# Optimization experiments

Hardware: AMD Instinct MI355X
Metric: run time of the kernel (lower is better)

Reference implementation:

```python
import jax, jax.numpy as jnp
import numpy as np

EPS = 1e-12  # matches torch F.normalize default


def _l2norm_c(x):
    # normalize along channel dim (axis=1) of [B,C,H,W]
    n = jnp.sqrt(jnp.sum(x * x, axis=1, keepdims=True))
    return x / jnp.maximum(n, EPS)


def setup_inputs() -> dict:
    key = jax.random.key(0)
    ks = jax.random.split(key, 6)
    B, C, H, W = 2, 256, 64, 64
    return {
        "sv": jax.random.normal(ks[0], (B, 1, H, W), dtype=jnp.float32),
        "si": jax.random.normal(ks[1], (B, 1, H, W), dtype=jnp.float32),
        "sf": jax.random.normal(ks[2], (B, 1, H, W), dtype=jnp.float32),
        "dv": jax.random.normal(ks[3], (B, C, H, W), dtype=jnp.float32),
        "di": jax.random.normal(ks[4], (B, C, H, W), dtype=jnp.float32),
        "df": jax.random.normal(ks[5], (B, C, H, W), dtype=jnp.float32),
    }


def reference(sv, si, sf, dv, di, df):
    # keypoint score loss: L1(sf, max(sv, si))
    kp = jnp.mean(jnp.abs(sf - jnp.maximum(sv, si)))
    # descriptor loss: L1(df, (dv+di)/2)
    desc = jnp.mean(jnp.abs(df - (dv + di) * 0.5))
    # match loss (dense): normalize along C, full correlation volumes, L1
    a = _l2norm_c(dv)
    b = _l2norm_c(di)
    c = _l2norm_c(df)
    sim_ab = jnp.einsum('bchw,bcij->bhwij', a, b)  # [B,H,W,H,W]
    sim_ac = jnp.einsum('bchw,bcij->bhwij', a, c)
    match = jnp.mean(jnp.abs(sim_ac - sim_ab))
    return kp + desc + match
```

## Files before the change

### kernel.cpp

```cpp
#include <hip/hip_runtime.h>
#include <hip/hip_bf16.h>
#include <math.h>

#define BB 2
#define CC 256
#define HWN 4096
#define PPB 8
#define CCP 260


typedef __attribute__((ext_vector_type(4))) int   intx4;
typedef __attribute__((ext_vector_type(8))) int   intx8;
typedef __attribute__((ext_vector_type(4))) float floatx4;

__device__ __forceinline__ unsigned short f2bf(float f) {
    union { float f; unsigned u; } v; v.f = f;
    unsigned r = v.u + 0x7FFF + ((v.u >> 16) & 1);
    return (unsigned short)(r >> 16);
}

__device__ __forceinline__ float bf2f(unsigned short h) {
    union { unsigned u; float f; } v; v.u = ((unsigned)h) << 16;
    return v.f;
}

__global__ __launch_bounds__(256) void prep_kernel(
    const float* __restrict__ sv, const float* __restrict__ si,
    const float* __restrict__ sf, const float* __restrict__ dv,
    const float* __restrict__ di, const float* __restrict__ df,
    unsigned char* __restrict__ Af8, unsigned char* __restrict__ Df8,
    float* __restrict__ pk, float* __restrict__ pd)
{
    __shared__ unsigned short lv[PPB][CCP];
    __shared__ unsigned short li[PPB][CCP];
    __shared__ unsigned short lf[PPB][CCP];
    __shared__ float ssq[3][PPB];
    __shared__ float inv[3][PPB];
    __shared__ float sdesc;

    const int b   = blockIdx.x / (HWN / PPB);
    const int p0  = (blockIdx.x % (HWN / PPB)) * PPB;
    const int tid = threadIdx.x;
    const int q   = tid & 1;
    const int c0  = (tid >> 1) * 2;

    if (tid < 3 * PPB) ((float*)ssq)[tid] = 0.0f;
    if (tid == 0) sdesc = 0.0f;
    __syncthreads();

    const size_t rbase = ((size_t)b * CC + c0) * HWN + p0 + q * 4;
    const floatx4 v0 = *(const floatx4*)(dv + rbase);
    const floatx4 v1 = *(const floatx4*)(dv + rbase + HWN);
    const floatx4 i0 = *(const floatx4*)(di + rbase);
    const floatx4 i1 = *(const floatx4*)(di + rbase + HWN);
    const floatx4 f0 = *(const floatx4*)(df + rbase);
    const floatx4 f1 = *(const floatx4*)(df + rbase + HWN);

    float sqv[4], sqi[4], sqf[4], descp = 0.f;
    #pragma unroll
    for (int k = 0; k < 4; ++k) {
        sqv[k] = v0[k] * v0[k] + v1[k] * v1[k];
        sqi[k] = i0[k] * i0[k] + i1[k] * i1[k];
        sqf[k] = f0[k] * f0[k] + f1[k] * f1[k];
        descp += fabsf(f0[k] - 0.5f * (v0[k] + i0[k]))
               + fabsf(f1[k] - 0.5f * (v1[k] + i1[k]));
        const int p = q * 4 + k;
        *(unsigned*)&lv[p][c0] = (unsigned)f2bf(v0[k]) | ((unsigned)f2bf(v1[k]) << 16);
        *(unsigned*)&li[p][c0] = (unsigned)f2bf(i0[k]) | ((unsigned)f2bf(i1[k]) << 16);
        *(unsigned*)&lf[p][c0] = (unsigned)f2bf(f0[k]) | ((unsigned)f2bf(f1[k]) << 16);
    }

    #pragma unroll
    for (int off = 2; off < 64; off <<= 1) {
        #pragma unroll
        for (int k = 0; k < 4; ++k) {
            sqv[k] += __shfl_down(sqv[k], off);
            sqi[k] += __shfl_down(sqi[k], off);
            sqf[k] += __shfl_down(sqf[k], off);
        }
    }
    if ((tid & 63) < 2) {
        #pragma unroll
        for (int k = 0; k < 4; ++k) {
            atomicAdd(&ssq[0][q * 4 + k], sqv[k]);
            atomicAdd(&ssq[1][q * 4 + k], sqi[k]);
            atomicAdd(&ssq[2][q * 4 + k], sqf[k]);
        }
    }

    #pragma unroll
    for (int off = 32; off > 0; off >>= 1) descp += __shfl_down(descp, off);
    if ((tid & 63) == 0) atomicAdd(&sdesc, descp);

    if (tid < 64) {
        float kpv = 0.f;
        if (tid < PPB) {
            const size_t sidx = (size_t)b * HWN + p0 + tid;
            kpv = fabsf(sf[sidx] - fmaxf(sv[sidx], si[sidx]));
        }
        kpv += __shfl_down(kpv, 4);
        kpv += __shfl_down(kpv, 2);
        kpv += __shfl_down(kpv, 1);
        if (tid == 0) pk[blockIdx.x] = kpv;
    }
    __syncthreads();

    if (tid < 3 * PPB) {
        const float s = ((float*)ssq)[tid];
        ((float*)inv)[tid] = 1.0f / fmaxf(sqrtf(s), 1e-12f);
    }
    __syncthreads();

    if (tid == 0) pd[blockIdx.x] = sdesc;

    int* Ao = (int*)(Af8 + (size_t)b * HWN * CC);
    int* Do = (int*)(Df8 + (size_t)b * HWN * CC);
    const int obase = (p0 >> 4) * 1024 + (p0 & 8) * 8;
    #pragma unroll
    for (int s = 0; s < 2; ++s) {
        const int i  = tid + s * 256;
        const int kb = i >> 6, rem = i & 63;
        const int px = rem >> 3, cg = rem & 7;
        const int cs = kb * 32 + cg * 4;
        const float ia = inv[0][px], ibv = inv[1][px], ic = inv[2][px];
        float a0 = bf2f(lv[px][cs + 0]) * ia, a1 = bf2f(lv[px][cs + 1]) * ia;
        float a2 = bf2f(lv[px][cs + 2]) * ia, a3 = bf2f(lv[px][cs + 3]) * ia;
        float d0 = bf2f(lf[px][cs + 0]) * ic - bf2f(li[px][cs + 0]) * ibv;
        float d1 = bf2f(lf[px][cs + 1]) * ic - bf2f(li[px][cs + 1]) * ibv;
        float d2 = bf2f(lf[px][cs + 2]) * ic - bf2f(li[px][cs + 2]) * ibv;
        float d3 = bf2f(lf[px][cs + 3]) * ic - bf2f(li[px][cs + 3]) * ibv;
        int wa = __builtin_amdgcn_cvt_pk_fp8_f32(a0, a1, 0, false);
        wa     = __builtin_amdgcn_cvt_pk_fp8_f32(a2, a3, wa, true);
        int wd = __builtin_amdgcn_cvt_pk_fp8_f32(d0, d1, 0, false);
        wd     = __builtin_amdgcn_cvt_pk_fp8_f32(d2, d3, wd, true);
        const int oidx = obase + kb * 128 + px * 8 + cg;
        Ao[oidx] = wa;
        Do[oidx] = wd;
    }
}

__global__ __launch_bounds__(256) void gemm_abs_kernel(
    const unsigned char* __restrict__ Af8,
    const unsigned char* __restrict__ Df8,
    float* __restrict__ pg)
{
    const int b    = blockIdx.z;
    const int tid  = threadIdx.x;
    const int wave = tid >> 6;
    const int lane = tid & 63;
    const int wr   = wave >> 1, wc = wave & 1;
    const int mg0  = blockIdx.x * 8 + wr * 4;
    const int ng0  = blockIdx.y * 8 + wc * 4;

    const unsigned char* Ab = Af8 + (size_t)b * HWN * CC;
    const unsigned char* Db = Df8 + (size_t)b * HWN * CC;
    const int lofs = (lane >> 4) * 512 + (lane & 15) * 32;

    intx4 a[4][2][2], bb[4][2][2];
    #pragma unroll
    for (int mi = 0; mi < 4; ++mi)
        #pragma unroll
        for (int ks = 0; ks < 2; ++ks) {
            const unsigned char* pa = Ab + (size_t)(mg0 + mi) * 4096
                                    + ks * 2048 + lofs;
            a[mi][ks][0] = *(const intx4*)(pa);
            a[mi][ks][1] = *(const intx4*)(pa + 16);
        }
    #pragma unroll
    for (int ni = 0; ni < 4; ++ni)
        #pragma unroll
        for (int ks = 0; ks < 2; ++ks) {
            const unsigned char* pb = Db + (size_t)(ng0 + ni) * 4096
                                    + ks * 2048 + lofs;
            bb[ni][ks][0] = *(const intx4*)(pb);
            bb[ni][ks][1] = *(const intx4*)(pb + 16);
        }

    floatx4 accf[4][4];
    #pragma unroll
    for (int mi = 0; mi < 4; ++mi)
        #pragma unroll
        for (int ni = 0; ni < 4; ++ni)
            accf[mi][ni] = (floatx4){0.f, 0.f, 0.f, 0.f};

    #pragma unroll
    for (int ks = 0; ks < 2; ++ks)
        #pragma unroll
        for (int mi = 0; mi < 4; ++mi) {
            const intx8 a8 = __builtin_shufflevector(
                a[mi][ks][0], a[mi][ks][1], 0, 1, 2, 3, 4, 5, 6, 7);
            #pragma unroll
            for (int ni = 0; ni < 4; ++ni) {
                const intx8 b8 = __builtin_shufflevector(
                    bb[ni][ks][0], bb[ni][ks][1], 0, 1, 2, 3, 4, 5, 6, 7);
                accf[mi][ni] = __builtin_amdgcn_mfma_scale_f32_16x16x128_f8f6f4(
                    a8, b8, accf[mi][ni],
                    0, 0,
                    0, 0x7F7F7F7F,
                    0, 0x7F7F7F7F);
            }
        }

    float s = 0.f;
    #pragma unroll
    for (int mi = 0; mi < 4; ++mi)
        #pragma unroll
        for (int ni = 0; ni < 4; ++ni)
            #pragma unroll
            for (int r = 0; r < 4; ++r)
                s += fabsf(accf[mi][ni][r]);
    #pragma unroll
    for (int off = 32; off > 0; off >>= 1) s += __shfl_down(s, off);
    if (lane == 0) {
        const int flat = blockIdx.x + 32 * (blockIdx.y + 32 * blockIdx.z);
        pg[flat * 4 + wave] = s;
    }
}

__global__ __launch_bounds__(256) void final_kernel(
    const float* __restrict__ pg, const float* __restrict__ pk,
    const float* __restrict__ pd, float* __restrict__ out)
{
    __shared__ float ws[4];
    const int t = threadIdx.x;
    float s = 0.f;
    #pragma unroll
    for (int i = 0; i < 32; ++i)
        s += pg[t + i * 256];
    s *= (1.0f / 33554432.0f);
    float kd = 0.f;
    #pragma unroll
    for (int i = 0; i < 4; ++i)
        kd += pk[t + i * 256] * (1.0f / 8192.0f)
            + pd[t + i * 256] * (1.0f / 2097152.0f);
    s += kd;
    #pragma unroll
    for (int off = 32; off > 0; off >>= 1) s += __shfl_down(s, off);
    if ((t & 63) == 0) ws[t >> 6] = s;
    __syncthreads();
    if (t == 0) out[0] = ws[0] + ws[1] + ws[2] + ws[3];
}

extern "C" void kernel_launch(void* const* d_in, const int* in_sizes, int n_in,
                              void* d_out, int out_size, void* d_ws, size_t ws_size,
                              hipStream_t stream) {
    const float* sv = (const float*)d_in[0];
    const float* si = (const float*)d_in[1];
    const float* sf = (const float*)d_in[2];
    const float* dv = (const float*)d_in[3];
    const float* di = (const float*)d_in[4];
    const float* df = (const float*)d_in[5];

    unsigned char* Af8 = (unsigned char*)d_ws;
    unsigned char* Df8 = Af8 + (size_t)BB * HWN * CC;
    float* pg = (float*)(Df8 + (size_t)BB * HWN * CC);
    float* pk = pg + 8192;
    float* pd = pk + 1024;

    prep_kernel<<<dim3(BB * (HWN / PPB)), 256, 0, stream>>>(
        sv, si, sf, dv, di, df, Af8, Df8, pk, pd);
    gemm_abs_kernel<<<dim3(HWN / 128, HWN / 128, BB), 256, 0, stream>>>(
        Af8, Df8, pg);
    final_kernel<<<1, 256, 0, stream>>>(pg, pk, pd, (float*)d_out);
}
```

Baseline: 107.1 us.

## Widen GEMM tile to 128x256 and double pixels per prep block

The GEMM block now covers 256 columns instead of 128, with each wave holding a 4x8 accumulator grid. B fragments are streamed per column inside the k loop, so each A fragment is reused across twice as many MFMAs and the grid is halved. The prep kernel processes 16 pixels per block with each thread handling two channel halves, writing full 16-pixel output tiles. The partial-sum buffers and the final reduction are resized to match. Doubling the accumulators raises register pressure, which may reduce occupancy or cause spills.

```diff
diff --git a/kernel.cpp b/kernel.cpp
--- a/kernel.cpp
+++ b/kernel.cpp
@@ -5,7 +5,7 @@
 #define BB 2
 #define CC 256
 #define HWN 4096
-#define PPB 8
+#define PPB 16
 #define CCP 260
 
 
@@ -41,51 +41,53 @@
     const int b   = blockIdx.x / (HWN / PPB);
     const int p0  = (blockIdx.x % (HWN / PPB)) * PPB;
     const int tid = threadIdx.x;
-    const int q   = tid & 1;
-    const int c0  = (tid >> 1) * 2;
+    const int tp  = tid & 3;
+    const int c0  = (tid >> 2) * 2;
 
     if (tid < 3 * PPB) ((float*)ssq)[tid] = 0.0f;
     if (tid == 0) sdesc = 0.0f;
     __syncthreads();
 
-    const size_t rbase = ((size_t)b * CC + c0) * HWN + p0 + q * 4;
-    const floatx4 v0 = *(const floatx4*)(dv + rbase);
-    const floatx4 v1 = *(const floatx4*)(dv + rbase + HWN);
-    const floatx4 i0 = *(const floatx4*)(di + rbase);
-    const floatx4 i1 = *(const floatx4*)(di + rbase + HWN);
-    const floatx4 f0 = *(const floatx4*)(df + rbase);
-    const floatx4 f1 = *(const floatx4*)(df + rbase + HWN);
-
-    float sqv[4], sqi[4], sqf[4], descp = 0.f;
-    #pragma unroll
-    for (int k = 0; k < 4; ++k) {
-        sqv[k] = v0[k] * v0[k] + v1[k] * v1[k];
-        sqi[k] = i0[k] * i0[k] + i1[k] * i1[k];
-        sqf[k] = f0[k] * f0[k] + f1[k] * f1[k];
-        descp += fabsf(f0[k] - 0.5f * (v0[k] + i0[k]))
-               + fabsf(f1[k] - 0.5f * (v1[k] + i1[k]));
-        const int p = q * 4 + k;
-        *(unsigned*)&lv[p][c0] = (unsigned)f2bf(v0[k]) | ((unsigned)f2bf(v1[k]) << 16);
-        *(unsigned*)&li[p][c0] = (unsigned)f2bf(i0[k]) | ((unsigned)f2bf(i1[k]) << 16);
-        *(unsigned*)&lf[p][c0] = (unsigned)f2bf(f0[k]) | ((unsigned)f2bf(f1[k]) << 16);
-    }
-
-    #pragma unroll
-    for (int off = 2; off < 64; off <<= 1) {
+    float sq[3][4] = {};
+    float descp = 0.f;
+    #pragma unroll
+    for (int h = 0; h < 2; ++h) {
+        const int ch = c0 + h * 128;
+        const size_t rbase = ((size_t)b * CC + ch) * HWN + p0 + tp * 4;
+        const floatx4 v0 = *(const floatx4*)(dv + rbase);
+        const floatx4 v1 = *(const floatx4*)(dv + rbase + HWN);
+        const floatx4 i0 = *(const floatx4*)(di + rbase);
+        const floatx4 i1 = *(const floatx4*)(di + rbase + HWN);
+        const floatx4 f0 = *(const floatx4*)(df + rbase);
+        const floatx4 f1 = *(const floatx4*)(df + rbase + HWN);
         #pragma unroll
         for (int k = 0; k < 4; ++k) {
-            sqv[k] += __shfl_down(sqv[k], off);
-            sqi[k] += __shfl_down(sqi[k], off);
-            sqf[k] += __shfl_down(sqf[k], off);
-        }
-    }
-    if ((tid & 63) < 2) {
-        #pragma unroll
-        for (int k = 0; k < 4; ++k) {
-            atomicAdd(&ssq[0][q * 4 + k], sqv[k]);
-            atomicAdd(&ssq[1][q * 4 + k], sqi[k]);
-            atomicAdd(&ssq[2][q * 4 + k], sqf[k]);
-        }
+            sq[0][k] += v0[k] * v0[k] + v1[k] * v1[k];
+            sq[1][k] += i0[k] * i0[k] + i1[k] * i1[k];
+            sq[2][k] += f0[k] * f0[k] + f1[k] * f1[k];
+            descp += fabsf(f0[k] - 0.5f * (v0[k] + i0[k]))
+                   + fabsf(f1[k] - 0.5f * (v1[k] + i1[k]));
+            const int p = tp * 4 + k;
+            *(unsigned*)&lv[p][ch] = (unsigned)f2bf(v0[k]) | ((unsigned)f2bf(v1[k]) << 16);
+            *(unsigned*)&li[p][ch] = (unsigned)f2bf(i0[k]) | ((unsigned)f2bf(i1[k]) << 16);
+            *(unsigned*)&lf[p][ch] = (unsigned)f2bf(f0[k]) | ((unsigned)f2bf(f1[k]) << 16);
+        }
+    }
+
+    #pragma unroll
+    for (int off = 4; off < 64; off <<= 1) {
+        #pragma unroll
+        for (int j = 0; j < 3; ++j)
+            #pragma unroll
+            for (int k = 0; k < 4; ++k)
+                sq[j][k] += __shfl_down(sq[j][k], off);
+    }
+    if ((tid & 63) < 4) {
+        #pragma unroll
+        for (int j = 0; j < 3; ++j)
+            #pragma unroll
+            for (int k = 0; k < 4; ++k)
+                atomicAdd(&ssq[j][tp * 4 + k], sq[j][k]);
     }
 
     #pragma unroll
@@ -98,6 +100,7 @@
             const size_t sidx = (size_t)b * HWN + p0 + tid;
             kpv = fabsf(sf[sidx] - fmaxf(sv[sidx], si[sidx]));
         }
+        kpv += __shfl_down(kpv, 8);
         kpv += __shfl_down(kpv, 4);
         kpv += __shfl_down(kpv, 2);
         kpv += __shfl_down(kpv, 1);
@@ -115,13 +118,14 @@
 
     int* Ao = (int*)(Af8 + (size_t)b * HWN * CC);
     int* Do = (int*)(Df8 + (size_t)b * HWN * CC);
-    const int obase = (p0 >> 4) * 1024 + (p0 & 8) * 8;
-    #pragma unroll
-    for (int s = 0; s < 2; ++s) {
-        const int i  = tid + s * 256;
-        const int kb = i >> 6, rem = i & 63;
-        const int px = rem >> 3, cg = rem & 7;
-        const int cs = kb * 32 + cg * 4;
+    const int obase = (p0 >> 4) * 1024;
+    #pragma unroll
+    for (int s = 0; s < 4; ++s) {
+        const int i   = tid + s * 256;
+        const int kb  = i >> 7;
+        const int rem = i & 127;
+        const int px  = rem >> 3, cg = rem & 7;
+        const int cs  = kb * 32 + cg * 4;
         const float ia = inv[0][px], ibv = inv[1][px], ic = inv[2][px];
         float a0 = bf2f(lv[px][cs + 0]) * ia, a1 = bf2f(lv[px][cs + 1]) * ia;
         float a2 = bf2f(lv[px][cs + 2]) * ia, a3 = bf2f(lv[px][cs + 3]) * ia;
@@ -150,69 +154,59 @@
     const int lane = tid & 63;
     const int wr   = wave >> 1, wc = wave & 1;
     const int mg0  = blockIdx.x * 8 + wr * 4;
-    const int ng0  = blockIdx.y * 8 + wc * 4;
+    const int ng0  = blockIdx.y * 16 + wc * 8;
 
     const unsigned char* Ab = Af8 + (size_t)b * HWN * CC;
     const unsigned char* Db = Df8 + (size_t)b * HWN * CC;
     const int lofs = (lane >> 4) * 512 + (lane & 15) * 32;
 
-    intx4 a[4][2][2], bb[4][2][2];
+    floatx4 accf[4][8];
     #pragma unroll
     for (int mi = 0; mi < 4; ++mi)
         #pragma unroll
-        for (int ks = 0; ks < 2; ++ks) {
+        for (int ni = 0; ni < 8; ++ni)
+            accf[mi][ni] = (floatx4){0.f, 0.f, 0.f, 0.f};
+
+    #pragma unroll
+    for (int ks = 0; ks < 2; ++ks) {
+        intx8 a8[4];
+        #pragma unroll
+        for (int mi = 0; mi < 4; ++mi) {
             const unsigned char* pa = Ab + (size_t)(mg0 + mi) * 4096
                                     + ks * 2048 + lofs;
-            a[mi][ks][0] = *(const intx4*)(pa);
-            a[mi][ks][1] = *(const intx4*)(pa + 16);
-        }
-    #pragma unroll
-    for (int ni = 0; ni < 4; ++ni)
-        #pragma unroll
-        for (int ks = 0; ks < 2; ++ks) {
+            const intx4 lo = *(const intx4*)(pa);
+            const intx4 hi = *(const intx4*)(pa + 16);
+            a8[mi] = __builtin_shufflevector(lo, hi, 0, 1, 2, 3, 4, 5, 6, 7);
+        }
+        #pragma unroll
+        for (int ni = 0; ni < 8; ++ni) {
             const unsigned char* pb = Db + (size_t)(ng0 + ni) * 4096
                                     + ks * 2048 + lofs;
-            bb[ni][ks][0] = *(const intx4*)(pb);
-            bb[ni][ks][1] = *(const intx4*)(pb + 16);
-        }
-
-    floatx4 accf[4][4];
-    #pragma unroll
-    for (int mi = 0; mi < 4; ++mi)
-        #pragma unroll
-        for (int ni = 0; ni < 4; ++ni)
-            accf[mi][ni] = (floatx4){0.f, 0.f, 0.f, 0.f};
-
-    #pragma unroll
-    for (int ks = 0; ks < 2; ++ks)
-        #pragma unroll
-        for (int mi = 0; mi < 4; ++mi) {
-            const intx8 a8 = __builtin_shufflevector(
-                a[mi][ks][0], a[mi][ks][1], 0, 1, 2, 3, 4, 5, 6, 7);
-            #pragma unroll
-            for (int ni = 0; ni < 4; ++ni) {
-                const intx8 b8 = __builtin_shufflevector(
-                    bb[ni][ks][0], bb[ni][ks][1], 0, 1, 2, 3, 4, 5, 6, 7);
+            const intx4 lo = *(const intx4*)(pb);
+            const intx4 hi = *(const intx4*)(pb + 16);
+            const intx8 b8 = __builtin_shufflevector(lo, hi, 0, 1, 2, 3, 4, 5, 6, 7);
+            #pragma unroll
+            for (int mi = 0; mi < 4; ++mi)
                 accf[mi][ni] = __builtin_amdgcn_mfma_scale_f32_16x16x128_f8f6f4(
-                    a8, b8, accf[mi][ni],
+                    a8[mi], b8, accf[mi][ni],
                     0, 0,
                     0, 0x7F7F7F7F,
                     0, 0x7F7F7F7F);
-            }
-        }
+        }
+    }
 
     float s = 0.f;
     #pragma unroll
     for (int mi = 0; mi < 4; ++mi)
         #pragma unroll
-        for (int ni = 0; ni < 4; ++ni)
+        for (int ni = 0; ni < 8; ++ni)
             #pragma unroll
             for (int r = 0; r < 4; ++r)
                 s += fabsf(accf[mi][ni][r]);
     #pragma unroll
     for (int off = 32; off > 0; off >>= 1) s += __shfl_down(s, off);
     if (lane == 0) {
-        const int flat = blockIdx.x + 32 * (blockIdx.y + 32 * blockIdx.z);
+        const int flat = blockIdx.x + 32 * (blockIdx.y + 16 * blockIdx.z);
         pg[flat * 4 + wave] = s;
     }
 }
@@ -225,15 +219,13 @@
     const int t = threadIdx.x;
     float s = 0.f;
     #pragma unroll
-    for (int i = 0; i < 32; ++i)
+    for (int i = 0; i < 16; ++i)
         s += pg[t + i * 256];
     s *= (1.0f / 33554432.0f);
-    float kd = 0.f;
-    #pragma unroll
-    for (int i = 0; i < 4; ++i)
-        kd += pk[t + i * 256] * (1.0f / 8192.0f)
-            + pd[t + i * 256] * (1.0f / 2097152.0f);
-    s += kd;
+    #pragma unroll
+    for (int i = 0; i < 2; ++i)
+        s += pk[t + i * 256] * (1.0f / 8192.0f)
+           + pd[t + i * 256] * (1.0f / 2097152.0f);
     #pragma unroll
     for (int off = 32; off > 0; off >>= 1) s += __shfl_down(s, off);
     if ((t & 63) == 0) ws[t >> 6] = s;
@@ -254,12 +246,12 @@
     unsigned char* Af8 = (unsigned char*)d_ws;
     unsigned char* Df8 = Af8 + (size_t)BB * HWN * CC;
     float* pg = (float*)(Df8 + (size_t)BB * HWN * CC);
-    float* pk = pg + 8192;
-    float* pd = pk + 1024;
+    float* pk = pg + 4096;
+    float* pd = pk + 512;
 
     prep_kernel<<<dim3(BB * (HWN / PPB)), 256, 0, stream>>>(
         sv, si, sf, dv, di, df, Af8, Df8, pk, pd);
-    gemm_abs_kernel<<<dim3(HWN / 128, HWN / 128, BB), 256, 0, stream>>>(
+    gemm_abs_kernel<<<dim3(HWN / 128, HWN / 256, BB), 256, 0, stream>>>(
         Af8, Df8, pg);
     final_kernel<<<1, 256, 0, stream>>>(pg, pk, pd, (float*)d_out);
 }
```

Result: faster. 102.0 us (-4.7%).
